# Optimization experiments

Measured on AMD Instinct MI355X. Metric: run time of the kernel, lower is better.

Reference implementation:

```python
import jax, jax.numpy as jnp
import numpy as np

EMB = 1024
HEADS = 16


def setup_inputs() -> dict:
    key = jax.random.key(0)
    k1, k2, k3, k4, k5 = jax.random.split(key, 5)
    b, n = 2, 2048
    x = jax.random.normal(k1, (b, n, EMB), dtype=jnp.float32)
    Wqkv = jax.random.normal(k2, (EMB, 3 * EMB), dtype=jnp.float32) * (EMB ** -0.5)
    bqkv = jax.random.normal(k3, (3 * EMB,), dtype=jnp.float32) * 0.02
    Wproj = jax.random.normal(k4, (EMB, EMB), dtype=jnp.float32) * (EMB ** -0.5)
    bproj = jax.random.normal(k5, (EMB,), dtype=jnp.float32) * 0.02
    return {"x": x, "Wqkv": Wqkv, "bqkv": bqkv, "Wproj": Wproj, "bproj": bproj}


def reference(x, Wqkv, bqkv, Wproj, bproj):
    b, n, e = x.shape
    h = HEADS
    d = e // h
    qkv = x @ Wqkv + bqkv                      # [b, n, 3e]
    # rearrange 'b n (h d qkv) -> qkv b h n d' : qkv index is innermost
    qkv = qkv.reshape(b, n, h, d, 3)
    qkv = jnp.transpose(qkv, (4, 0, 2, 1, 3))  # [3, b, h, n, d]
    q, k, v = qkv[0], qkv[1], qkv[2]
    energy = jnp.einsum('bhqd,bhkd->bhqk', q, k)
    scaling = jnp.float32(e) ** 0.5            # NOTE: sqrt(emb_size), not head_dim
    att = jax.nn.softmax(energy / scaling, axis=-1)
    out = jnp.einsum('bhql,bhld->bhqd', att, v)
    out = jnp.transpose(out, (0, 2, 1, 3)).reshape(b, n, e)  # 'b h n d -> b n (h d)'
    return out @ Wproj + bproj
```

## Files before the change

kernel.cpp:

```cpp
#include <hip/hip_runtime.h>
#include <hip/hip_bf16.h>
#include <stdint.h>

typedef __bf16 bf16;
typedef __attribute__((ext_vector_type(8))) __bf16 bf16x8;
typedef __attribute__((ext_vector_type(4))) __bf16 bf16x4;
typedef __attribute__((ext_vector_type(4))) float f32x4;
typedef __attribute__((ext_vector_type(16))) float f32x16;

#define MFMA16(a, b, c) __builtin_amdgcn_mfma_f32_16x16x32_bf16((a), (b), (c), 0, 0, 0)
#define MFMA32(a, b, c) __builtin_amdgcn_mfma_f32_32x32x16_bf16((a), (b), (c), 0, 0, 0)

#define QSCALE 0.045084220027780106f

__device__ __forceinline__ void glds16(const void* g, void* l) {
  __builtin_amdgcn_global_load_lds(
      (const __attribute__((address_space(1))) void*)g,
      (__attribute__((address_space(3))) void*)l, 16, 0, 0);
}

__device__ __forceinline__ bf16x8 ldsfrag(const unsigned char* base, int row, int colb) {
  return *(const bf16x8*)(base + row * 128 + (colb ^ ((row & 7) << 4)));
}

__device__ __forceinline__ uint32_t pkbf16(float a, float b) {
  uint32_t r;
  asm("v_cvt_pk_bf16_f32 %0, %1, %2" : "=v"(r) : "v"(a), "v"(b));
  return r;
}

__device__ __forceinline__ float fexp2(float x) {
#if __has_builtin(__builtin_amdgcn_exp2f)
  return __builtin_amdgcn_exp2f(x);
#else
  float r;
  asm("v_exp_f32 %0, %1" : "=v"(r) : "v"(x));
  return r;
#endif
}

__device__ __forceinline__ f32x16 zero16() {
  f32x16 v;
#pragma unroll
  for (int i = 0; i < 16; ++i) v[i] = 0.f;
  return v;
}

__global__ __launch_bounds__(256) void k_prep_x(const float* __restrict__ x, bf16* __restrict__ xb) {
  int gid = blockIdx.x * 256 + threadIdx.x;
  const f32x4* xv = (const f32x4*)x;
  f32x4 a = xv[(size_t)gid * 2], b = xv[(size_t)gid * 2 + 1];
  bf16x8 o;
#pragma unroll
  for (int i = 0; i < 4; ++i) { o[i] = (bf16)a[i]; o[i + 4] = (bf16)b[i]; }
  *(bf16x8*)(xb + (size_t)gid * 8) = o;
}

template <int MODE>
__global__ __launch_bounds__(256) void k_prep_w(const float* __restrict__ W, bf16* __restrict__ WT) {
  __shared__ float tile[64][256];
  const int C = (MODE == 0) ? 3072 : 1024;
  const int c0 = blockIdx.x * 256, k0 = blockIdx.y * 64;
  const int lw = threadIdx.x & 63, w = threadIdx.x >> 6;
#pragma unroll
  for (int i = 0; i < 16; ++i) {
    int r = i * 4 + w;
    f32x4 v = *(const f32x4*)(W + (size_t)(k0 + r) * C + c0 + lw * 4);
    *(f32x4*)&tile[r][lw * 4] = v;
  }
  __syncthreads();
  const int c = c0 + threadIdx.x;
  int j;
  float sc = 1.0f;
  if (MODE == 0) {
    int h = c / 192, rem = c - h * 192, dd = rem / 3, wh = rem - dd * 3;
    j = wh * 1024 + h * 64 + dd;
    if (wh == 0) sc = QSCALE;
  } else {
    j = c;
  }
#pragma unroll
  for (int ch = 0; ch < 8; ++ch) {
    bf16x8 o;
#pragma unroll
    for (int i = 0; i < 8; ++i) o[i] = (bf16)(tile[ch * 8 + i][threadIdx.x] * sc);
    *(bf16x8*)(WT + (size_t)j * 1024 + k0 + ch * 8) = o;
  }
}

__global__ __launch_bounds__(256) void k_prep_bias(const float* __restrict__ bqkv, float* __restrict__ bp) {
  int gid = blockIdx.x * 256 + threadIdx.x;
  int wj = gid >> 10, rr = gid & 1023, hh = rr >> 6, d2 = rr & 63;
  float v = bqkv[hh * 192 + d2 * 3 + wj];
  bp[gid] = (wj == 0) ? v * QSCALE : v;
}

template <int EPI>
__global__ __launch_bounds__(256) void k_gemm(const bf16* __restrict__ A, const bf16* __restrict__ BT,
                                              const float* __restrict__ bias, bf16* __restrict__ qk,
                                              bf16* __restrict__ vt, float* __restrict__ outf) {
  __shared__ __align__(16) unsigned char sA[16384];
  __shared__ __align__(16) unsigned char sB[16384];
  const int tid = threadIdx.x;
  const int l = tid & 63, w = tid >> 6, g = l >> 4, l15 = l & 15;
  const int wr = w >> 1, wc = w & 1;
  const int bm = blockIdx.y, bn = blockIdx.x;
  const unsigned char* Ab = (const unsigned char*)A + (size_t)bm * 128 * 2048;
  const unsigned char* Bb = (const unsigned char*)BT + (size_t)bn * 128 * 2048;
  f32x4 acc[4][4];
#pragma unroll
  for (int mi = 0; mi < 4; ++mi)
#pragma unroll
    for (int ni = 0; ni < 4; ++ni) acc[mi][ni] = (f32x4){0.f, 0.f, 0.f, 0.f};

  for (int kt = 0; kt < 16; ++kt) {
    const int k0b = kt * 128;
#pragma unroll
    for (int p = 0; p < 4; ++p) {
      int co = (p * 256 + tid) * 16;
      int row = co >> 7, wb = co & 127;
      int sw = wb ^ ((row & 7) << 4);
      glds16(Ab + (size_t)row * 2048 + k0b + sw, sA + co);
      glds16(Bb + (size_t)row * 2048 + k0b + sw, sB + co);
    }
    __syncthreads();
#pragma unroll
    for (int ks = 0; ks < 2; ++ks) {
      bf16x8 af[4], bfr[4];
#pragma unroll
      for (int mi = 0; mi < 4; ++mi) af[mi] = ldsfrag(sA, wr * 64 + mi * 16 + l15, ks * 64 + g * 16);
#pragma unroll
      for (int ni = 0; ni < 4; ++ni) bfr[ni] = ldsfrag(sB, wc * 64 + ni * 16 + l15, ks * 64 + g * 16);
      __builtin_amdgcn_s_setprio(1);
#pragma unroll
      for (int mi = 0; mi < 4; ++mi)
#pragma unroll
        for (int ni = 0; ni < 4; ++ni) acc[mi][ni] = MFMA16(af[mi], bfr[ni], acc[mi][ni]);
      __builtin_amdgcn_s_setprio(0);
    }
    __syncthreads();
  }
#pragma unroll
  for (int ni = 0; ni < 4; ++ni) {
    int j = bn * 128 + wc * 64 + ni * 16 + l15;
    float bj = bias[j];
#pragma unroll
    for (int mi = 0; mi < 4; ++mi) {
      int m0 = bm * 128 + wr * 64 + mi * 16 + g * 4;
      float v[4];
#pragma unroll
      for (int rr = 0; rr < 4; ++rr) v[rr] = acc[mi][ni][rr] + bj;
      if (EPI == 0) {
        int which = j >> 10, r = j & 1023, h = r >> 6, dd = r & 63;
        int b = m0 >> 11, nn = m0 & 2047;
        if (which < 2) {
#pragma unroll
          for (int rr = 0; rr < 4; ++rr)
            qk[(size_t)which * 4194304 + (((size_t)b * 16 + h) * 2048 + nn + rr) * 64 + dd] = (bf16)v[rr];
        } else {
          bf16x4 pw = {(bf16)v[0], (bf16)v[1], (bf16)v[2], (bf16)v[3]};
          *(bf16x4*)(vt + (((size_t)b * 16 + h) * 64 + dd) * 2048 + nn) = pw;
        }
      } else {
#pragma unroll
        for (int rr = 0; rr < 4; ++rr) outf[(size_t)(m0 + rr) * 1024 + j] = v[rr];
      }
    }
  }
}

__global__ __launch_bounds__(512, 1) void k_attn(const bf16* __restrict__ Qg, const bf16* __restrict__ Kg,
                                                 const bf16* __restrict__ VTg, bf16* __restrict__ Og) {
  __shared__ __align__(16) unsigned char smem[67584];
  const int tid = threadIdx.x;
  const int l = tid & 63, w = tid >> 6;
  const int q = l & 31, hi = l >> 5;
  const int g = w >> 2, wl = w & 3;
  const int stid = tid & 255;

  const int bid = blockIdx.x;
  const int wg = (bid & 7) * 32 + (bid >> 3);
  const int bh = wg >> 3;
  const int q0w = (wg & 7) * 256 + wl * 64;

  bf16x8 qf[2][4];
#pragma unroll
  for (int qt = 0; qt < 2; ++qt)
#pragma unroll
    for (int ks = 0; ks < 4; ++ks)
      qf[qt][ks] = *(const bf16x8*)(Qg + ((size_t)bh * 2048 + q0w + qt * 32 + q) * 64 + ks * 16 + hi * 8);

  f32x16 oacc[2][2];
#pragma unroll
  for (int qt = 0; qt < 2; ++qt) { oacc[qt][0] = zero16(); oacc[qt][1] = zero16(); }
  float lrun4[2][4] = {{0.f, 0.f, 0.f, 0.f}, {0.f, 0.f, 0.f, 0.f}};
  bf16x8 pb[2][4];

  const unsigned char* Kb = (const unsigned char*)Kg + (size_t)bh * 262144 + (size_t)g * 131072;
  const unsigned char* Vb = (const unsigned char*)VTg + (size_t)bh * 262144 + (size_t)g * 2048;
  unsigned char* sKg = smem + g * 16384;
  unsigned char* sVg = smem + 32768 + g * 16384;

  const int co0 = stid * 16, co1 = (256 + stid) * 16;
  const int row0 = co0 >> 7, row1 = co1 >> 7;
  const int sw0 = (co0 & 127) ^ ((row0 & 7) << 4), sw1 = (co1 & 127) ^ ((row1 & 7) << 4);

#define STAGE_K(kb_, buf_)                                                        \
  do {                                                                            \
    const unsigned char* Ksrc = Kb + (size_t)(kb_) * 8192;                        \
    glds16(Ksrc + (co0 & ~127) + sw0, sKg + (buf_) * 8192 + co0);                 \
    glds16(Ksrc + (co1 & ~127) + sw1, sKg + (buf_) * 8192 + co1);                 \
  } while (0)
#define STAGE_V(kb_, buf_)                                                        \
  do {                                                                            \
    glds16(Vb + (size_t)row0 * 4096 + (size_t)(kb_) * 128 + sw0, sVg + (buf_) * 8192 + co0); \
    glds16(Vb + (size_t)row1 * 4096 + (size_t)(kb_) * 128 + sw1, sVg + (buf_) * 8192 + co1); \
  } while (0)

#define QK_EXP_PACK(kbase_)                                                       \
  do {                                                                            \
    _Pragma("unroll") for (int kt = 0; kt < 2; ++kt) {                            \
      bf16x8 kf[4];                                                               \
      _Pragma("unroll") for (int ks = 0; ks < 4; ++ks)                            \
        kf[ks] = ldsfrag((kbase_), kt * 32 + q, ks * 32 + hi * 16);               \
      _Pragma("unroll") for (int qt = 0; qt < 2; ++qt) {                          \
        f32x16 sacc = zero16();                                                   \
        __builtin_amdgcn_s_setprio(1);                                            \
        _Pragma("unroll") for (int ks = 0; ks < 4; ++ks)                          \
          sacc = MFMA32(kf[ks], qf[qt][ks], sacc);                                \
        __builtin_amdgcn_s_setprio(0);                                            \
        float pe[16];                                                             \
        _Pragma("unroll") for (int r = 0; r < 16; ++r) pe[r] = fexp2(sacc[r]);    \
        _Pragma("unroll") for (int m = 0; m < 4; ++m)                             \
          _Pragma("unroll") for (int j = 0; j < 4; ++j) lrun4[qt][j] += pe[4 * m + j]; \
        uint32_t c[4][2];                                                         \
        _Pragma("unroll") for (int m = 0; m < 4; ++m) {                           \
          c[m][0] = pkbf16(pe[4 * m], pe[4 * m + 1]);                             \
          c[m][1] = pkbf16(pe[4 * m + 2], pe[4 * m + 3]);                         \
        }                                                                         \
        _Pragma("unroll") for (int s = 0; s < 2; ++s) {                           \
          uint32_t x0 = c[2 * s][0], y0 = c[2 * s + 1][0];                        \
          uint32_t x1 = c[2 * s][1], y1 = c[2 * s + 1][1];                        \
          asm("v_permlane32_swap_b32 %0, %1" : "+v"(x0), "+v"(y0));               \
          asm("v_permlane32_swap_b32 %0, %1" : "+v"(x1), "+v"(y1));               \
          union { uint32_t u[4]; bf16x8 v; } bfr;                                 \
          bfr.u[0] = x0; bfr.u[1] = x1; bfr.u[2] = y0; bfr.u[3] = y1;             \
          pb[qt][kt * 2 + s] = bfr.v;                                             \
        }                                                                         \
      }                                                                           \
    }                                                                             \
  } while (0)

#define PV_TILE(vbase_)                                                           \
  do {                                                                            \
    __builtin_amdgcn_s_setprio(1);                                                \
    _Pragma("unroll") for (int ks = 0; ks < 4; ++ks)                              \
      _Pragma("unroll") for (int dt = 0; dt < 2; ++dt) {                          \
        bf16x8 vf = ldsfrag((vbase_), dt * 32 + q, ks * 32 + hi * 16);            \
        _Pragma("unroll") for (int qt = 0; qt < 2; ++qt)                          \
          oacc[qt][dt] = MFMA32(vf, pb[qt][ks], oacc[qt][dt]);                    \
      }                                                                           \
    __builtin_amdgcn_s_setprio(0);                                                \
  } while (0)

  STAGE_K(0, 0);
  STAGE_V(0, 0);
  __syncthreads();
  STAGE_K(1, 1);
  QK_EXP_PACK(sKg);
  __syncthreads();
  int cur = 0;

  for (int kb = 0; kb < 15; ++kb) {
    const int nxt = cur ^ 1;
    if (kb < 14) STAGE_K(kb + 2, cur);
    STAGE_V(kb + 1, nxt);
    PV_TILE(sVg + cur * 8192);
    QK_EXP_PACK(sKg + nxt * 8192);
    __syncthreads();
    cur = nxt;
  }
  PV_TILE(sVg + cur * 8192);

#undef STAGE_K
#undef STAGE_V
#undef QK_EXP_PACK
#undef PV_TILE

  float lrun[2];
#pragma unroll
  for (int qt = 0; qt < 2; ++qt)
    lrun[qt] = (lrun4[qt][0] + lrun4[qt][1]) + (lrun4[qt][2] + lrun4[qt][3]);

  float* mbuf = (float*)smem;
  float* lb = (float*)(smem + 65536);
  if (g == 1) {
#pragma unroll
    for (int qt = 0; qt < 2; ++qt) {
#pragma unroll
      for (int dt = 0; dt < 2; ++dt)
#pragma unroll
        for (int r = 0; r < 16; ++r)
          mbuf[((wl * 64 + qt * 32 + dt * 16 + r) << 6) + l] = oacc[qt][dt][r];
      lb[(wl * 2 + qt) * 64 + l] = lrun[qt];
    }
  }
  __syncthreads();
  if (g == 0) {
#pragma unroll
    for (int qt = 0; qt < 2; ++qt)
#pragma unroll
      for (int dt = 0; dt < 2; ++dt)
#pragma unroll
        for (int r = 0; r < 16; ++r)
          oacc[qt][dt][r] += mbuf[((wl * 64 + qt * 32 + dt * 16 + r) << 6) + l];
  }
  __syncthreads();
  if (g == 0) {
    const int b = bh >> 4, h = bh & 15;
    unsigned char* sO = smem + 32768 + wl * 4096;
#pragma unroll
    for (int qt = 0; qt < 2; ++qt) {
      float lr = lrun[qt] + lb[(wl * 2 + qt) * 64 + l];
      float ps = lr + __shfl_xor(lr, 32);
      float linv = 1.0f / ps;
#pragma unroll
      for (int dt = 0; dt < 2; ++dt)
#pragma unroll
        for (int m = 0; m < 4; ++m) {
          uint32_t b0 = pkbf16(oacc[qt][dt][4 * m] * linv, oacc[qt][dt][4 * m + 1] * linv);
          uint32_t b1 = pkbf16(oacc[qt][dt][4 * m + 2] * linv, oacc[qt][dt][4 * m + 3] * linv);
          int byteo = (dt * 64 + m * 16 + hi * 8) ^ ((q & 7) << 4);
          uint32_t* dst = (uint32_t*)(sO + q * 128 + byteo);
          dst[0] = b0; dst[1] = b1;
        }
      const int q0 = q0w + qt * 32;
#pragma unroll
      for (int rd = 0; rd < 4; ++rd) {
        int byteo = hi * 64 + rd * 16;
        bf16x8 v = *(const bf16x8*)(sO + q * 128 + (byteo ^ ((q & 7) << 4)));
        *(bf16x8*)(Og + ((size_t)b * 2048 + q0 + q) * 1024 + h * 64 + byteo / 2) = v;
      }
    }
  }
}

extern "C" void kernel_launch(void* const* d_in, const int* in_sizes, int n_in,
                              void* d_out, int out_size, void* d_ws, size_t ws_size,
                              hipStream_t stream) {
  const float* x = (const float*)d_in[0];
  const float* Wqkv = (const float*)d_in[1];
  const float* bqkv = (const float*)d_in[2];
  const float* Wproj = (const float*)d_in[3];
  const float* bproj = (const float*)d_in[4];
  float* out = (float*)d_out;
  char* ws = (char*)d_ws;

  bf16* XB = (bf16*)(ws + 0);
  bf16* WQT = (bf16*)(ws + 8388608);
  float* BQP = (float*)(ws + 14680064);
  bf16* WPT = (bf16*)(ws + 14696448);
  bf16* Q = (bf16*)(ws + 16793600);
  bf16* K = (bf16*)(ws + 25182208);
  bf16* VT = (bf16*)(ws + 33570816);
  bf16* AO = XB;
  (void)K;
  (void)ws_size;

  k_prep_x<<<2048, 256, 0, stream>>>(x, XB);
  k_prep_w<0><<<dim3(12, 16), 256, 0, stream>>>(Wqkv, WQT);
  k_prep_w<1><<<dim3(4, 16), 256, 0, stream>>>(Wproj, WPT);
  k_prep_bias<<<12, 256, 0, stream>>>(bqkv, BQP);
  k_gemm<0><<<dim3(24, 32), 256, 0, stream>>>(XB, WQT, BQP, Q, VT, nullptr);
  k_attn<<<256, 512, 0, stream>>>(Q, Q + 4194304, VT, AO);
  k_gemm<1><<<dim3(8, 32), 256, 0, stream>>>(AO, WPT, bproj, nullptr, nullptr, out);
}
```

Baseline: 123.6 us.

## Triple-buffer K/V in LDS with explicit vmcnt waits and raw barriers

The attention kernel's K/V staging moves from double to triple buffering in LDS, and the main loop is unrolled by six with ping-pong P register sets. Each iteration now waits with a partial s_waitcnt vmcnt and uses a raw s_barrier instead of __syncthreads. This lets global-to-LDS loads run further ahead and stop stalling on all outstanding loads, at the cost of more LDS per block, more registers for the extra P fragments, and hand-tuned wait counts that must stay exact.

```diff
diff --git a/kernel.cpp b/kernel.cpp
--- a/kernel.cpp
+++ b/kernel.cpp
@@ -171,7 +171,7 @@
 
 __global__ __launch_bounds__(512, 1) void k_attn(const bf16* __restrict__ Qg, const bf16* __restrict__ Kg,
                                                  const bf16* __restrict__ VTg, bf16* __restrict__ Og) {
-  __shared__ __align__(16) unsigned char smem[67584];
+  __shared__ __align__(16) unsigned char smem[100352];
   const int tid = threadIdx.x;
   const int l = tid & 63, w = tid >> 6;
   const int q = l & 31, hi = l >> 5;
@@ -194,12 +194,12 @@
 #pragma unroll
   for (int qt = 0; qt < 2; ++qt) { oacc[qt][0] = zero16(); oacc[qt][1] = zero16(); }
   float lrun4[2][4] = {{0.f, 0.f, 0.f, 0.f}, {0.f, 0.f, 0.f, 0.f}};
-  bf16x8 pb[2][4];
+  bf16x8 pbA[2][4], pbB[2][4];
 
   const unsigned char* Kb = (const unsigned char*)Kg + (size_t)bh * 262144 + (size_t)g * 131072;
   const unsigned char* Vb = (const unsigned char*)VTg + (size_t)bh * 262144 + (size_t)g * 2048;
-  unsigned char* sKg = smem + g * 16384;
-  unsigned char* sVg = smem + 32768 + g * 16384;
+  unsigned char* sKg = smem + g * 24576;
+  unsigned char* sVg = smem + 49152 + g * 24576;
 
   const int co0 = stid * 16, co1 = (256 + stid) * 16;
   const int row0 = co0 >> 7, row1 = co1 >> 7;
@@ -217,7 +217,19 @@
     glds16(Vb + (size_t)row1 * 4096 + (size_t)(kb_) * 128 + sw1, sVg + (buf_) * 8192 + co1); \
   } while (0)
 
-#define QK_EXP_PACK(kbase_)                                                       \
+#define VMWAIT(n)                                                                 \
+  do {                                                                            \
+    asm volatile("s_waitcnt vmcnt(" #n ")" ::: "memory");                         \
+    __builtin_amdgcn_sched_barrier(0);                                            \
+  } while (0)
+#define RAWBAR()                                                                  \
+  do {                                                                            \
+    __builtin_amdgcn_sched_barrier(0);                                            \
+    __builtin_amdgcn_s_barrier();                                                 \
+    __builtin_amdgcn_sched_barrier(0);                                            \
+  } while (0)
+
+#define QK_EXP_PACK(kbase_, PBOUT)                                                \
   do {                                                                            \
     _Pragma("unroll") for (int kt = 0; kt < 2; ++kt) {                            \
       bf16x8 kf[4];                                                               \
@@ -245,47 +257,67 @@
           asm("v_permlane32_swap_b32 %0, %1" : "+v"(x1), "+v"(y1));               \
           union { uint32_t u[4]; bf16x8 v; } bfr;                                 \
           bfr.u[0] = x0; bfr.u[1] = x1; bfr.u[2] = y0; bfr.u[3] = y1;             \
-          pb[qt][kt * 2 + s] = bfr.v;                                             \
+          PBOUT[qt][kt * 2 + s] = bfr.v;                                          \
         }                                                                         \
       }                                                                           \
     }                                                                             \
   } while (0)
 
-#define PV_TILE(vbase_)                                                           \
+#define PV_TILE(vbase_, PB)                                                       \
   do {                                                                            \
     __builtin_amdgcn_s_setprio(1);                                                \
     _Pragma("unroll") for (int ks = 0; ks < 4; ++ks)                              \
       _Pragma("unroll") for (int dt = 0; dt < 2; ++dt) {                          \
         bf16x8 vf = ldsfrag((vbase_), dt * 32 + q, ks * 32 + hi * 16);            \
-        _Pragma("unroll") for (int qt = 0; qt < 2; ++qt)                          \
-          oacc[qt][dt] = MFMA32(vf, pb[qt][ks], oacc[qt][dt]);                    \
+        _Pragma("unroll") for (int qtp = 0; qtp < 2; ++qtp)                       \
+          oacc[qtp][dt] = MFMA32(vf, PB[qtp][ks], oacc[qtp][dt]);                 \
       }                                                                           \
     __builtin_amdgcn_s_setprio(0);                                                \
   } while (0)
 
+#define ITER(T, KR, VR, KS, VS, DOKS, DOVS, PBIN, PBOUT, VM)                      \
+  do {                                                                            \
+    if (DOKS) STAGE_K((T) + 3, KS);                                               \
+    if (DOVS) STAGE_V((T) + 2, VS);                                               \
+    PV_TILE(sVg + (VR) * 8192, PBIN);                                             \
+    QK_EXP_PACK(sKg + (KR) * 8192, PBOUT);                                        \
+    VMWAIT(VM);                                                                   \
+    RAWBAR();                                                                     \
+  } while (0)
+
   STAGE_K(0, 0);
   STAGE_V(0, 0);
-  __syncthreads();
   STAGE_K(1, 1);
-  QK_EXP_PACK(sKg);
-  __syncthreads();
-  int cur = 0;
-
-  for (int kb = 0; kb < 15; ++kb) {
-    const int nxt = cur ^ 1;
-    if (kb < 14) STAGE_K(kb + 2, cur);
-    STAGE_V(kb + 1, nxt);
-    PV_TILE(sVg + cur * 8192);
-    QK_EXP_PACK(sKg + nxt * 8192);
-    __syncthreads();
-    cur = nxt;
-  }
-  PV_TILE(sVg + cur * 8192);
+  STAGE_V(1, 1);
+  STAGE_K(2, 2);
+  VMWAIT(6);
+  RAWBAR();
+  QK_EXP_PACK(sKg, pbA);
+  VMWAIT(2);
+  RAWBAR();
+
+  for (int t0 = 0; t0 < 12; t0 += 6) {
+    ITER(t0 + 0, 1, 0, 0, 2, 1, 1, pbA, pbB, 4);
+    ITER(t0 + 1, 2, 1, 1, 0, 1, 1, pbB, pbA, 4);
+    ITER(t0 + 2, 0, 2, 2, 1, 1, 1, pbA, pbB, 4);
+    ITER(t0 + 3, 1, 0, 0, 2, 1, 1, pbB, pbA, 4);
+    ITER(t0 + 4, 2, 1, 1, 0, 1, 1, pbA, pbB, 4);
+    ITER(t0 + 5, 0, 2, 2, 1, 1, 1, pbB, pbA, 4);
+  }
+  ITER(12, 1, 0, 0, 2, 1, 1, pbA, pbB, 4);
+  ITER(13, 2, 1, 1, 0, 0, 1, pbB, pbA, 2);
+  ITER(14, 0, 2, 2, 1, 0, 0, pbA, pbB, 0);
+  PV_TILE(sVg + 0 * 8192, pbB);
 
 #undef STAGE_K
 #undef STAGE_V
+#undef VMWAIT
+#undef RAWBAR
 #undef QK_EXP_PACK
 #undef PV_TILE
+#undef ITER
+
+  __syncthreads();
 
   float lrun[2];
 #pragma unroll
@@ -293,7 +325,7 @@
     lrun[qt] = (lrun4[qt][0] + lrun4[qt][1]) + (lrun4[qt][2] + lrun4[qt][3]);
 
   float* mbuf = (float*)smem;
-  float* lb = (float*)(smem + 65536);
+  float* lb = (float*)(smem + 98304);
   if (g == 1) {
 #pragma unroll
     for (int qt = 0; qt < 2; ++qt) {
@@ -318,7 +350,7 @@
   __syncthreads();
   if (g == 0) {
     const int b = bh >> 4, h = bh & 15;
-    unsigned char* sO = smem + 32768 + wl * 4096;
+    unsigned char* sO = smem + 65536 + wl * 4096;
 #pragma unroll
     for (int qt = 0; qt < 2; ++qt) {
       float lr = lrun[qt] + lb[(wl * 2 + qt) * 64 + l];
```

New measurement: 139.7 us. 1.13x slower.
